# Kernel optimization log

Hardware: AMD Instinct MI355X
Metric: run time of the kernel (lower is better)

## Reference

```python
import math
import jax, jax.numpy as jnp
import numpy as np

P_NEW = 10000  # module init: new=10000


def _design_filter(p_full=10000, q_full=48000, L=10, beta=5.0):
    """Octave-style anti-alias FIR: kaiser-windowed sinc, normalized to sum 1
    (the module stores window = h / sum(h))."""
    g = math.gcd(p_full, q_full)
    p, q = p_full // g, q_full // g          # 5, 24
    order = 2 * L * max(p, q)                # 480 -> 481 taps (odd)
    t = np.arange(-order // 2, order // 2 + 1)
    cutoff = 1.0 / (2 * max(p, q))           # normalized cycles/sample
    h = 2 * cutoff * np.sinc(2 * cutoff * t) * np.kaiser(order + 1, beta)
    h = h / np.sum(h)
    return h.astype(np.float32)


def setup_inputs() -> dict:
    key = jax.random.key(0)
    B, T = 32, 1440000  # 32 channels, 30 s @ 48 kHz
    x = jax.random.normal(key, (B, T), dtype=jnp.float32)
    h = jnp.asarray(_design_filter())  # [481]
    return {"x": x, "h": h, "orig_fs": 48000}


def reference(x, h, orig_fs):
    # resample_poly: upsample by `up` (zero-insert), FIR filter, decimate by `down`
    up, down = P_NEW, int(orig_fs)
    g = math.gcd(up, down)
    up //= g
    down //= g                                   # 5, 24 for 48 kHz
    if up == 1 and down == 1:
        return x

    half_len = (h.shape[0] - 1) // 2
    h = h * up                                   # gain compensation
    n_in = x.shape[-1]

    n_pre_pad = (down - half_len % down) % down
    h_padded = jnp.pad(h, (n_pre_pad, 0))
    filt_len = h_padded.shape[0]
    h_flipped = jnp.flip(h_padded)[None, None, :]  # OIH

    x_flat = x.reshape(-1, 1, n_in)                # NCH
    # lhs_dilation=up == zero-stuffed upsample; torch pads filt_len-1 both sides
    # and the torch x_up carries (up-1) trailing zeros -> extra right pad.
    # window_strides=down == the y[..., ::down] decimation, computed without waste.
    y_down = jax.lax.conv_general_dilated(
        x_flat, h_flipped,
        window_strides=(down,),
        padding=[(filt_len - 1, filt_len - 1 + up - 1)],
        lhs_dilation=(up,),
        dimension_numbers=("NCH", "OIH", "NCH"),
    )

    n_out = n_in * up // down + (1 if (n_in * up) % down else 0)
    n_pre_remove = (half_len + n_pre_pad) // down
    y = y_down[..., n_pre_remove:n_pre_remove + n_out]
    return y.reshape(x.shape[:-1] + (n_out,))
```

## Files before the change

kernel.cpp:

```cpp
#include <hip/hip_runtime.h>


#define NIN    1440000
#define NOUTR  300000
#define NROWS  32
#define KTOT   60000
#define NCHUNK 938
#define S      8
#define NBX    118
#define TILE_E 1632
#define TILE_P 1648
#define NT8    204

typedef __attribute__((ext_vector_type(8))) short short8v;
typedef __attribute__((ext_vector_type(4))) float float4v;

__device__ __forceinline__ unsigned short f2b(float f) {
    unsigned u = __builtin_bit_cast(unsigned, f);
    u += 0x7fff + ((u >> 16) & 1);
    return (unsigned short)(u >> 16);
}

__global__ void prep_taps_kernel(const float* __restrict__ h,
                                 unsigned short* __restrict__ Bpk) {
    int i = blockIdx.x * blockDim.x + threadIdx.x;
    if (i < 2048) {
        int j = i & 7, l = (i >> 3) & 63, m = i >> 9;
        int d = l & 15, q = l >> 4;
        int c = 32 * m + 8 * q + j;
        int t = 24 * d + 480 - 5 * c;
        float v = (d < 5 && t >= 0 && t <= 480) ? h[t] * 5.0f : 0.0f;
        Bpk[i] = f2b(v);
    }
}

__global__ __launch_bounds__(256, 7) void resample_kernel(
    const float* __restrict__ x, const unsigned short* __restrict__ Bpk,
    float* __restrict__ y)
{
    __shared__ short ldsb[2][TILE_P];
    const int tid  = threadIdx.x;
    const int lane = tid & 63;
    const int wv   = tid >> 6;
    const int row  = blockIdx.y;
    const int cb   = blockIdx.x * S;
    const int n    = min(S, NCHUNK - cb);
    const float* __restrict__ xr = x + (size_t)row * NIN;

    const short8v B0 = *reinterpret_cast<const short8v*>(Bpk + (0 * 64 + lane) * 8);
    const short8v B1 = *reinterpret_cast<const short8v*>(Bpk + (1 * 64 + lane) * 8);
    const short8v B2 = *reinterpret_cast<const short8v*>(Bpk + (2 * 64 + lane) * 8);
    const short8v B3 = *reinterpret_cast<const short8v*>(Bpk + (3 * 64 + lane) * 8);

    if (tid < 16) {
        ldsb[0][TILE_E + tid] = 0;
        ldsb[1][TILE_E + tid] = 0;
    }

    float4 pa, pb;

    auto load_regs = [&](int c) {
        const int g0 = 1536 * c - 48;
        if (tid < NT8) {
            if (g0 >= 0 && g0 + TILE_E <= NIN) {
                const float4* __restrict__ p = reinterpret_cast<const float4*>(xr + g0);
                pa = p[2 * tid];
                pb = p[2 * tid + 1];
            } else {
                float v[8];
                #pragma unroll
                for (int j = 0; j < 8; ++j) {
                    const int g = g0 + 8 * tid + j;
                    v[j] = ((unsigned)g < NIN) ? xr[g] : 0.0f;
                }
                pa = make_float4(v[0], v[1], v[2], v[3]);
                pb = make_float4(v[4], v[5], v[6], v[7]);
            }
        }
    };

    auto write_buf = [&](int b) {
        if (tid < NT8) {
            unsigned r0, r1, r2, r3;
            asm("v_cvt_pk_bf16_f32 %0, %1, %2" : "=v"(r0) : "v"(pa.x), "v"(pa.y));
            asm("v_cvt_pk_bf16_f32 %0, %1, %2" : "=v"(r1) : "v"(pa.z), "v"(pa.w));
            asm("v_cvt_pk_bf16_f32 %0, %1, %2" : "=v"(r2) : "v"(pb.x), "v"(pb.y));
            asm("v_cvt_pk_bf16_f32 %0, %1, %2" : "=v"(r3) : "v"(pb.z), "v"(pb.w));
            *reinterpret_cast<uint4*>(&ldsb[b][8 * tid]) = make_uint4(r0, r1, r2, r3);
        }
    };

    load_regs(cb);
    write_buf(0);
    __syncthreads();

    for (int s = 0; s < n; ++s) {
        if (s + 1 < n) load_regs(cb + s + 1);

        const int r = lane & 15, q = lane >> 4;
        const short* __restrict__ ap = &ldsb[s & 1][24 * (16 * wv + r) + 8 * q];
        const short8v A0 = *reinterpret_cast<const short8v*>(ap);
        const short8v A1 = *reinterpret_cast<const short8v*>(ap + 32);
        const short8v A2 = *reinterpret_cast<const short8v*>(ap + 64);
        const short8v A3 = *reinterpret_cast<const short8v*>(ap + 96);

        float4v acc = {0.f, 0.f, 0.f, 0.f};
        acc = __builtin_amdgcn_mfma_f32_16x16x32_bf16(A0, B0, acc, 0, 0, 0);
        acc = __builtin_amdgcn_mfma_f32_16x16x32_bf16(A1, B1, acc, 0, 0, 0);
        acc = __builtin_amdgcn_mfma_f32_16x16x32_bf16(A2, B2, acc, 0, 0, 0);
        acc = __builtin_amdgcn_mfma_f32_16x16x32_bf16(A3, B3, acc, 0, 0, 0);

        const int d = lane & 15;
        if (d < 5) {
            const int kbase = 64 * (cb + s) + 16 * wv + 4 * q;
            float* __restrict__ yr = y + (size_t)row * NOUTR;
            #pragma unroll
            for (int j = 0; j < 4; ++j) {
                const int k = kbase + j;
                if (k < KTOT) yr[5 * (size_t)k + d] = acc[j];
            }
        }

        if (s + 1 < n) write_buf((s + 1) & 1);
        __syncthreads();
    }
}

extern "C" void kernel_launch(void* const* d_in, const int* in_sizes, int n_in,
                              void* d_out, int out_size, void* d_ws, size_t ws_size,
                              hipStream_t stream) {
    const float* x = (const float*)d_in[0];
    const float* h = (const float*)d_in[1];
    float* y = (float*)d_out;
    unsigned short* Bpk = (unsigned short*)d_ws;

    prep_taps_kernel<<<8, 256, 0, stream>>>(h, Bpk);
    dim3 grid(NBX, NROWS);
    resample_kernel<<<grid, 256, 0, stream>>>(x, Bpk, y);
}
```

Measured before the change: 44.05 us.

## Replace per-block chunk loop with one chunk per block

Each block now handles a single 1536-sample chunk, replacing the previous loop over 8 chunks with a double-buffered LDS prefetch. The grid grows from 118 to 938 blocks per row, so more waves are resident to hide global-memory latency, and the double-buffer and loop overhead go away. In exchange, each block pays its own launch, B-fragment loads and the halo overlap, and there is no longer any in-block overlap between loading and computing.

Measured after the change: 48.70 us. +10.6%, slower.

```diff
diff --git a/kernel.cpp b/kernel.cpp
--- a/kernel.cpp
+++ b/kernel.cpp
@@ -6,8 +6,6 @@
 #define NROWS  32
 #define KTOT   60000
 #define NCHUNK 938
-#define S      8
-#define NBX    118
 #define TILE_E 1632
 #define TILE_P 1648
 #define NT8    204
@@ -38,91 +36,69 @@
     const float* __restrict__ x, const unsigned short* __restrict__ Bpk,
     float* __restrict__ y)
 {
-    __shared__ short ldsb[2][TILE_P];
+    __shared__ short ldsb[TILE_P];
     const int tid  = threadIdx.x;
     const int lane = tid & 63;
     const int wv   = tid >> 6;
     const int row  = blockIdx.y;
-    const int cb   = blockIdx.x * S;
-    const int n    = min(S, NCHUNK - cb);
+    const int ct   = blockIdx.x;
     const float* __restrict__ xr = x + (size_t)row * NIN;
+    const int g0 = 1536 * ct - 48;
 
     const short8v B0 = *reinterpret_cast<const short8v*>(Bpk + (0 * 64 + lane) * 8);
     const short8v B1 = *reinterpret_cast<const short8v*>(Bpk + (1 * 64 + lane) * 8);
     const short8v B2 = *reinterpret_cast<const short8v*>(Bpk + (2 * 64 + lane) * 8);
     const short8v B3 = *reinterpret_cast<const short8v*>(Bpk + (3 * 64 + lane) * 8);
 
-    if (tid < 16) {
-        ldsb[0][TILE_E + tid] = 0;
-        ldsb[1][TILE_E + tid] = 0;
+    if (tid < TILE_P - TILE_E) ldsb[TILE_E + tid] = 0;
+
+    if (tid < NT8) {
+        float4 pa, pb;
+        if (g0 >= 0 && g0 + TILE_E <= NIN) {
+            const float4* __restrict__ p = reinterpret_cast<const float4*>(xr + g0);
+            pa = p[2 * tid];
+            pb = p[2 * tid + 1];
+        } else {
+            float v[8];
+            #pragma unroll
+            for (int j = 0; j < 8; ++j) {
+                const int g = g0 + 8 * tid + j;
+                v[j] = ((unsigned)g < NIN) ? xr[g] : 0.0f;
+            }
+            pa = make_float4(v[0], v[1], v[2], v[3]);
+            pb = make_float4(v[4], v[5], v[6], v[7]);
+        }
+        unsigned r0, r1, r2, r3;
+        asm("v_cvt_pk_bf16_f32 %0, %1, %2" : "=v"(r0) : "v"(pa.x), "v"(pa.y));
+        asm("v_cvt_pk_bf16_f32 %0, %1, %2" : "=v"(r1) : "v"(pa.z), "v"(pa.w));
+        asm("v_cvt_pk_bf16_f32 %0, %1, %2" : "=v"(r2) : "v"(pb.x), "v"(pb.y));
+        asm("v_cvt_pk_bf16_f32 %0, %1, %2" : "=v"(r3) : "v"(pb.z), "v"(pb.w));
+        *reinterpret_cast<uint4*>(&ldsb[8 * tid]) = make_uint4(r0, r1, r2, r3);
     }
-
-    float4 pa, pb;
-
-    auto load_regs = [&](int c) {
-        const int g0 = 1536 * c - 48;
-        if (tid < NT8) {
-            if (g0 >= 0 && g0 + TILE_E <= NIN) {
-                const float4* __restrict__ p = reinterpret_cast<const float4*>(xr + g0);
-                pa = p[2 * tid];
-                pb = p[2 * tid + 1];
-            } else {
-                float v[8];
-                #pragma unroll
-                for (int j = 0; j < 8; ++j) {
-                    const int g = g0 + 8 * tid + j;
-                    v[j] = ((unsigned)g < NIN) ? xr[g] : 0.0f;
-                }
-                pa = make_float4(v[0], v[1], v[2], v[3]);
-                pb = make_float4(v[4], v[5], v[6], v[7]);
-            }
-        }
-    };
-
-    auto write_buf = [&](int b) {
-        if (tid < NT8) {
-            unsigned r0, r1, r2, r3;
-            asm("v_cvt_pk_bf16_f32 %0, %1, %2" : "=v"(r0) : "v"(pa.x), "v"(pa.y));
-            asm("v_cvt_pk_bf16_f32 %0, %1, %2" : "=v"(r1) : "v"(pa.z), "v"(pa.w));
-            asm("v_cvt_pk_bf16_f32 %0, %1, %2" : "=v"(r2) : "v"(pb.x), "v"(pb.y));
-            asm("v_cvt_pk_bf16_f32 %0, %1, %2" : "=v"(r3) : "v"(pb.z), "v"(pb.w));
-            *reinterpret_cast<uint4*>(&ldsb[b][8 * tid]) = make_uint4(r0, r1, r2, r3);
-        }
-    };
-
-    load_regs(cb);
-    write_buf(0);
     __syncthreads();
 
-    for (int s = 0; s < n; ++s) {
-        if (s + 1 < n) load_regs(cb + s + 1);
+    const int r = lane & 15, q = lane >> 4;
+    const short* __restrict__ ap = &ldsb[24 * (16 * wv + r) + 8 * q];
+    const short8v A0 = *reinterpret_cast<const short8v*>(ap);
+    const short8v A1 = *reinterpret_cast<const short8v*>(ap + 32);
+    const short8v A2 = *reinterpret_cast<const short8v*>(ap + 64);
+    const short8v A3 = *reinterpret_cast<const short8v*>(ap + 96);
 
-        const int r = lane & 15, q = lane >> 4;
-        const short* __restrict__ ap = &ldsb[s & 1][24 * (16 * wv + r) + 8 * q];
-        const short8v A0 = *reinterpret_cast<const short8v*>(ap);
-        const short8v A1 = *reinterpret_cast<const short8v*>(ap + 32);
-        const short8v A2 = *reinterpret_cast<const short8v*>(ap + 64);
-        const short8v A3 = *reinterpret_cast<const short8v*>(ap + 96);
+    float4v acc = {0.f, 0.f, 0.f, 0.f};
+    acc = __builtin_amdgcn_mfma_f32_16x16x32_bf16(A0, B0, acc, 0, 0, 0);
+    acc = __builtin_amdgcn_mfma_f32_16x16x32_bf16(A1, B1, acc, 0, 0, 0);
+    acc = __builtin_amdgcn_mfma_f32_16x16x32_bf16(A2, B2, acc, 0, 0, 0);
+    acc = __builtin_amdgcn_mfma_f32_16x16x32_bf16(A3, B3, acc, 0, 0, 0);
 
-        float4v acc = {0.f, 0.f, 0.f, 0.f};
-        acc = __builtin_amdgcn_mfma_f32_16x16x32_bf16(A0, B0, acc, 0, 0, 0);
-        acc = __builtin_amdgcn_mfma_f32_16x16x32_bf16(A1, B1, acc, 0, 0, 0);
-        acc = __builtin_amdgcn_mfma_f32_16x16x32_bf16(A2, B2, acc, 0, 0, 0);
-        acc = __builtin_amdgcn_mfma_f32_16x16x32_bf16(A3, B3, acc, 0, 0, 0);
-
-        const int d = lane & 15;
-        if (d < 5) {
-            const int kbase = 64 * (cb + s) + 16 * wv + 4 * q;
-            float* __restrict__ yr = y + (size_t)row * NOUTR;
-            #pragma unroll
-            for (int j = 0; j < 4; ++j) {
-                const int k = kbase + j;
-                if (k < KTOT) yr[5 * (size_t)k + d] = acc[j];
-            }
+    const int d = lane & 15;
+    if (d < 5) {
+        const int kbase = 64 * ct + 16 * wv + 4 * q;
+        float* __restrict__ yr = y + (size_t)row * NOUTR;
+        #pragma unroll
+        for (int j = 0; j < 4; ++j) {
+            const int k = kbase + j;
+            if (k < KTOT) yr[5 * (size_t)k + d] = acc[j];
         }
-
-        if (s + 1 < n) write_buf((s + 1) & 1);
-        __syncthreads();
     }
 }
 
@@ -135,6 +111,6 @@
     unsigned short* Bpk = (unsigned short*)d_ws;
 
     prep_taps_kernel<<<8, 256, 0, stream>>>(h, Bpk);
-    dim3 grid(NBX, NROWS);
+    dim3 grid(NCHUNK, NROWS);
     resample_kernel<<<grid, 256, 0, stream>>>(x, Bpk, y);
 }
```
